# Kernel optimization log

Measured on AMD Instinct MI355X. Metric: run time of the kernel, lower is better.

## Reference

```python
import jax, jax.numpy as jnp
import numpy as np

N_HEAD = 16

def setup_inputs() -> dict:
    key = jax.random.key(0)
    ks = jax.random.split(key, 9)
    B, T, C = 4, 2048, 1024
    s = 0.02
    return {
        "x": jax.random.normal(ks[0], (B, T, C), dtype=jnp.float32),
        "Wq": jax.random.normal(ks[1], (C, C), dtype=jnp.float32) * s,
        "bq": jnp.zeros((C,), dtype=jnp.float32),
        "Wk": jax.random.normal(ks[2], (C, C), dtype=jnp.float32) * s,
        "bk": jnp.zeros((C,), dtype=jnp.float32),
        "Wv": jax.random.normal(ks[3], (C, C), dtype=jnp.float32) * s,
        "bv": jnp.zeros((C,), dtype=jnp.float32),
        "Wo": jax.random.normal(ks[4], (C, C), dtype=jnp.float32) * s,
        "bo": jnp.zeros((C,), dtype=jnp.float32),
    }

def reference(x, Wq, bq, Wk, bk, Wv, bv, Wo, bo):
    B, T, C = x.shape
    H = N_HEAD
    d = C // H
    # QKV projections (Linear: y = x @ W + b), split heads -> [B, H, T, d]
    def proj(W, b):
        return (x @ W + b).reshape(B, T, H, d).transpose(0, 2, 1, 3)
    q = proj(Wq, bq)
    k = proj(Wk, bk)
    v = proj(Wv, bv)
    scale = jnp.float32(d) ** -0.5
    scores = jnp.einsum("bhtd,bhsd->bhts", q, k) * scale  # [B,H,T,T]
    attn = jax.nn.softmax(scores, axis=-1)
    out = jnp.einsum("bhts,bhsd->bhtd", attn, v)  # [B,H,T,d]
    out = out.transpose(0, 2, 1, 3).reshape(B, T, C)
    return out @ Wo + bo
```

## Files before the change

kernel.cpp:

```cpp
#include <hip/hip_runtime.h>
#include <hip/hip_bf16.h>

typedef unsigned short u16;
typedef unsigned int   u32;

typedef __bf16 bf16x8 __attribute__((ext_vector_type(8)));
typedef float  f32x4  __attribute__((ext_vector_type(4)));

#define MFMA16(A, B, C) __builtin_amdgcn_mfma_f32_16x16x32_bf16(A, B, C, 0, 0, 0)

static __device__ __forceinline__ u16 f2bf(float f) {
  union { float f; u32 u; } v; v.f = f;
  u32 r = v.u + 0x7fffu + ((v.u >> 16) & 1u);
  return (u16)(r >> 16);
}

static __device__ __forceinline__ float exp2a(float x) {
  float r; asm("v_exp_f32 %0, %1" : "=v"(r) : "v"(x)); return r;
}
static __device__ __forceinline__ float max3f(float a, float b, float c) {
  float r; asm("v_max3_f32 %0, %1, %2, %3" : "=v"(r) : "v"(a), "v"(b), "v"(c)); return r;
}
static __device__ __forceinline__ u32 cvtpk(float lo, float hi) {
  u32 r; asm("v_cvt_pk_bf16_f32 %0, %1, %2" : "=v"(r) : "v"(lo), "v"(hi)); return r;
}

static __device__ __forceinline__ void async16(const void* g, void* l) {
  __builtin_amdgcn_global_load_lds((const __attribute__((address_space(1))) void*)g,
                                   (__attribute__((address_space(3))) void*)l, 16, 0, 0);
}

static __device__ __forceinline__ int permrow(int r) {
  return (r & 3) | (((r >> 3) & 1) << 2);
}

__global__ __launch_bounds__(256) void cvtx_k(const float* __restrict__ x, u16* __restrict__ xb) {
  size_t i = ((size_t)blockIdx.x * 256 + threadIdx.x) * 4;
  float4 v = *(const float4*)(x + i);
  u32 lo = (u32)f2bf(v.x) | ((u32)f2bf(v.y) << 16);
  u32 hi = (u32)f2bf(v.z) | ((u32)f2bf(v.w) << 16);
  *(uint2*)(xb + i) = make_uint2(lo, hi);
}

__global__ __launch_bounds__(256) void wt_k(const float* __restrict__ Wq, const float* __restrict__ Wk,
                                            const float* __restrict__ Wv, const float* __restrict__ Wo,
                                            u16* __restrict__ WT) {
  const int z = blockIdx.z;
  const float* W = (z == 0) ? Wq : (z == 1) ? Wk : (z == 2) ? Wv : Wo;
  u16* out = WT + (size_t)z * 1048576;
  __shared__ float tile[32][33];
  const int tx = threadIdx.x & 31, ty = threadIdx.x >> 5;
  const int n0 = blockIdx.x * 32, k0 = blockIdx.y * 32;
#pragma unroll
  for (int i = 0; i < 4; i++)
    tile[ty + i * 8][tx] = W[(size_t)(k0 + ty + i * 8) * 1024 + n0 + tx];
  __syncthreads();
#pragma unroll
  for (int i = 0; i < 4; i++)
    out[(size_t)(n0 + ty + i * 8) * 1024 + k0 + tx] = f2bf(tile[tx][ty + i * 8]);
}

template <int MODE>
__global__ __launch_bounds__(256) void gemm_k(const u16* __restrict__ A, const u16* __restrict__ WTall,
                                              const float* __restrict__ b0, const float* __restrict__ b1,
                                              const float* __restrict__ b2,
                                              u16* __restrict__ outb, float* __restrict__ outf) {
  __shared__ u16 As[128 * 32];
  __shared__ u16 Bs[128 * 32];
  const int tid = threadIdx.x;
  const int m0 = blockIdx.x * 128;
  const int n0 = blockIdx.y * 128;
  const int z = blockIdx.z;
  const u16* WT = WTall + (size_t)(MODE == 0 ? z : 3) * 1048576;
  const float* bias = (MODE == 0) ? (z == 0 ? b0 : (z == 1 ? b1 : b2)) : b0;
  const float scl = (MODE == 0 && z == 0) ? 0.18033688011112042f : 1.0f;

  const int lane = tid & 63;
  const int wid = tid >> 6;
  const int wr = wid >> 1, wc = wid & 1;
  const int g = lane >> 4, cc = lane & 15;

  const int srow = tid >> 2;
  const int scol = (tid & 3) * 8;
  const u16* gA0 = A + (size_t)(m0 + srow) * 1024 + scol;
  const u16* gA1 = A + (size_t)(m0 + srow + 64) * 1024 + scol;
  const u16* gB0 = WT + (size_t)(n0 + srow) * 1024 + scol;
  const u16* gB1 = WT + (size_t)(n0 + srow + 64) * 1024 + scol;
  u16* lA0 = &As[tid * 8]; u16* lA1 = &As[2048 + tid * 8];
  u16* lB0 = &Bs[tid * 8]; u16* lB1 = &Bs[2048 + tid * 8];

  f32x4 acc[4][4] = {};

  for (int kb = 0; kb < 1024; kb += 32) {
    __syncthreads();
    async16(gA0 + kb, lA0);
    async16(gA1 + kb, lA1);
    async16(gB0 + kb, lB0);
    async16(gB1 + kb, lB1);
    __syncthreads();
    bf16x8 af[4], bfv[4];
#pragma unroll
    for (int i = 0; i < 4; i++)
      af[i] = *(const bf16x8*)&As[(wr * 64 + i * 16 + cc) * 32 + g * 8];
#pragma unroll
    for (int i = 0; i < 4; i++)
      bfv[i] = *(const bf16x8*)&Bs[(wc * 64 + i * 16 + cc) * 32 + g * 8];
#pragma unroll
    for (int mi = 0; mi < 4; mi++)
#pragma unroll
      for (int ni = 0; ni < 4; ni++)
        acc[mi][ni] = MFMA16(af[mi], bfv[ni], acc[mi][ni]);
  }

#pragma unroll
  for (int mi = 0; mi < 4; mi++) {
#pragma unroll
    for (int ni = 0; ni < 4; ni++) {
      const int n = n0 + wc * 64 + ni * 16 + cc;
      const float bn = bias[n];
      const int mb = m0 + wr * 64 + mi * 16 + g * 4;
      if (MODE == 0) {
        u16* o = outb + (size_t)z * 8388608;
        if (z == 2) {
          u16 h[4];
#pragma unroll
          for (int r = 0; r < 4; r++) h[r] = f2bf(acc[mi][ni][r] + bn);
          const size_t idx = ((size_t)(((mb >> 11) * 16 + (n >> 6)) * 64 + (n & 63))) * 2048 + (mb & 2047);
          *(uint2*)&o[idx] = make_uint2((u32)h[0] | ((u32)h[1] << 16), (u32)h[2] | ((u32)h[3] << 16));
        } else {
#pragma unroll
          for (int r = 0; r < 4; r++) {
            const int m = mb + r;
            const float val = (acc[mi][ni][r] + bn) * scl;
            o[((size_t)((m >> 11) * 16 + (n >> 6)) * 2048 + (m & 2047)) * 64 + (n & 63)] = f2bf(val);
          }
        }
      } else {
#pragma unroll
        for (int r = 0; r < 4; r++)
          outf[(size_t)(mb + r) * 1024 + n] = acc[mi][ni][r] + bn;
      }
    }
  }
}

#define SOFTMAX_GRP(ST, MRUN, O, PF)                                          \
  {                                                                           \
    float pm_ = max3f(max3f(ST[0][0], ST[0][1], ST[0][2]),                    \
                      max3f(ST[0][3], ST[1][0], ST[1][1]),                    \
                      fmaxf(ST[1][2], ST[1][3]));                             \
    if (!__all(pm_ <= MRUN + 8.0f)) {                                         \
      pm_ = fmaxf(pm_, __shfl_xor(pm_, 16));                                  \
      pm_ = fmaxf(pm_, __shfl_xor(pm_, 32));                                  \
      const float mn_ = fmaxf(MRUN, pm_);                                     \
      const float al_ = exp2a(MRUN - mn_);                                    \
      _Pragma("unroll")                                                       \
      for (int r_ = 0; r_ < 4; ++r_) {                                        \
        const float ar_ = __shfl(al_, g * 4 + r_);                            \
        _Pragma("unroll")                                                     \
        for (int t_ = 0; t_ < 5; ++t_) O[t_][r_] *= ar_;                      \
      }                                                                       \
      MRUN = mn_;                                                             \
    }                                                                         \
    const float e0_ = exp2a(ST[0][0] - MRUN), e1_ = exp2a(ST[0][1] - MRUN);   \
    const float e2_ = exp2a(ST[0][2] - MRUN), e3_ = exp2a(ST[0][3] - MRUN);   \
    const float e4_ = exp2a(ST[1][0] - MRUN), e5_ = exp2a(ST[1][1] - MRUN);   \
    const float e6_ = exp2a(ST[1][2] - MRUN), e7_ = exp2a(ST[1][3] - MRUN);   \
    union { u32 u[4]; bf16x8 v; } pu_;                                        \
    pu_.u[0] = cvtpk(e0_, e1_); pu_.u[1] = cvtpk(e2_, e3_);                   \
    pu_.u[2] = cvtpk(e4_, e5_); pu_.u[3] = cvtpk(e6_, e7_);                   \
    PF = pu_.v;                                                               \
  }

#define COMPUTE(BUF)                                                          \
  _Pragma("unroll")                                                           \
  for (int sub = 0; sub < 2; ++sub) {                                         \
    f32x4 stA[2], stB[2];                                                     \
    _Pragma("unroll")                                                         \
    for (int i = 0; i < 2; ++i) {                                             \
      const int row_ = sub * 32 + 8 * a_ + 4 * i + b_;                        \
      const int sl_ = g ^ permrow(row_);                                      \
      bf16x8 k0 = *(const bf16x8*)&Ks[BUF][row_ * 64 + (sl_ << 3)];           \
      bf16x8 k1 = *(const bf16x8*)&Ks[BUF][row_ * 64 + ((sl_ ^ 4) << 3)];     \
      f32x4 t0 = {};                                                          \
      t0 = MFMA16(k0, qfA[0], t0); t0 = MFMA16(k1, qfA[1], t0); stA[i] = t0;  \
      f32x4 t1 = {};                                                          \
      t1 = MFMA16(k0, qfB[0], t1); t1 = MFMA16(k1, qfB[1], t1); stB[i] = t1;  \
    }                                                                         \
    bf16x8 pfA, pfB;                                                          \
    SOFTMAX_GRP(stA, mA, oA, pfA);                                            \
    SOFTMAX_GRP(stB, mB, oB, pfB);                                            \
    _Pragma("unroll")                                                         \
    for (int t = 0; t < 4; ++t) {                                             \
      const int vrow_ = t * 16 + cc;                                          \
      const int sv_ = (sub * 4 + g) ^ permrow(vrow_);                         \
      bf16x8 vf = *(const bf16x8*)&Vs[BUF][vrow_ * 64 + (sv_ << 3)];          \
      oA[t] = MFMA16(pfA, vf, oA[t]);                                         \
      oB[t] = MFMA16(pfB, vf, oB[t]);                                         \
    }                                                                         \
    oA[4] = MFMA16(pfA, vone, oA[4]);                                         \
    oB[4] = MFMA16(pfB, vone, oB[4]);                                         \
  }

#define STEP(BUF, IT)                                                         \
  {                                                                           \
    __syncthreads();                                                          \
    if ((IT) < 31) {                                                          \
      const size_t ko_ = (size_t)((IT) + 1) * 4096;                           \
      const size_t vo_ = (size_t)((IT) + 1) * 64;                             \
      async16(kS0 + ko_, &Ks[BUF ^ 1][tid * 8]);                              \
      async16(kS1 + ko_, &Ks[BUF ^ 1][tid * 8 + 2048]);                       \
      async16(vS0 + vo_, &Vs[BUF ^ 1][tid * 8]);                              \
      async16(vS1 + vo_, &Vs[BUF ^ 1][tid * 8 + 2048]);                       \
    }                                                                         \
    COMPUTE(BUF)                                                              \
  }

__global__ __launch_bounds__(256) void attn_k(const u16* __restrict__ Qg, const u16* __restrict__ Kg,
                                              const u16* __restrict__ Vtg, u16* __restrict__ ctx) {
  __shared__ u16 Ks[2][4096];
  __shared__ u16 Vs[2][4096];
  const int tid = threadIdx.x;
  const int lane = tid & 63;
  const int wid = tid >> 6;
  const int g = lane >> 4, cc = lane & 15;
  const int a_ = cc >> 2, b_ = cc & 3;
  const int bh = blockIdx.y;
  const int q0 = blockIdx.x * 128 + wid * 16;
  const size_t base = (size_t)bh * 131072;

  bf16x8 qfA[2], qfB[2];
#pragma unroll
  for (int c2 = 0; c2 < 2; c2++) {
    qfA[c2] = *(const bf16x8*)(Qg + base + (size_t)(q0 + cc) * 64 + c2 * 32 + g * 8);
    qfB[c2] = *(const bf16x8*)(Qg + base + (size_t)(q0 + 64 + cc) * 64 + c2 * 32 + g * 8);
  }

  bf16x8 vone;
#pragma unroll
  for (int j = 0; j < 8; j++) vone[j] = (__bf16)1.0f;

  float mA = -30000.0f, mB = -30000.0f;
  f32x4 oA[5] = {}, oB[5] = {};

  const int r0 = tid >> 3, r1 = r0 + 32;
  const int slot = tid & 7;
  const int sp0 = slot ^ permrow(r0), sp1 = slot ^ permrow(r1);
  const u16* kS0 = Kg + base + (size_t)r0 * 64 + (sp0 << 3);
  const u16* kS1 = Kg + base + (size_t)r1 * 64 + (sp1 << 3);
  const u16* vS0 = Vtg + base + (size_t)r0 * 2048 + (sp0 << 3);
  const u16* vS1 = Vtg + base + (size_t)r1 * 2048 + (sp1 << 3);

  async16(kS0, &Ks[0][tid * 8]);
  async16(kS1, &Ks[0][tid * 8 + 2048]);
  async16(vS0, &Vs[0][tid * 8]);
  async16(vS1, &Vs[0][tid * 8 + 2048]);

  for (int it = 0; it < 32; it += 2) {
    STEP(0, it)
    STEP(1, it + 1)
  }

  const int b = bh >> 4, h = bh & 15;
#pragma unroll
  for (int r = 0; r < 4; r++) {
    {
      const float inv = __builtin_amdgcn_rcpf(oA[4][r]);
      const int q = q0 + g * 4 + r;
#pragma unroll
      for (int t = 0; t < 4; t++)
        ctx[((size_t)((b * 2048 + q) * 16 + h)) * 64 + t * 16 + cc] = f2bf(oA[t][r] * inv);
    }
    {
      const float inv = __builtin_amdgcn_rcpf(oB[4][r]);
      const int q = q0 + 64 + g * 4 + r;
#pragma unroll
      for (int t = 0; t < 4; t++)
        ctx[((size_t)((b * 2048 + q) * 16 + h)) * 64 + t * 16 + cc] = f2bf(oB[t][r] * inv);
    }
  }
}

extern "C" void kernel_launch(void* const* d_in, const int* in_sizes, int n_in,
                              void* d_out, int out_size, void* d_ws, size_t ws_size,
                              hipStream_t stream) {
  const float* x  = (const float*)d_in[0];
  const float* Wq = (const float*)d_in[1];
  const float* bq = (const float*)d_in[2];
  const float* Wk = (const float*)d_in[3];
  const float* bk = (const float*)d_in[4];
  const float* Wv = (const float*)d_in[5];
  const float* bv = (const float*)d_in[6];
  const float* Wo = (const float*)d_in[7];
  const float* bo = (const float*)d_in[8];
  float* out = (float*)d_out;

  char* w = (char*)d_ws;
  u16* xb   = (u16*)(w);
  u16* WT   = (u16*)(w + (16u << 20));
  u16* QKV  = (u16*)(w + (24u << 20));
  u16* ctxb = (u16*)(w + (72u << 20));

  cvtx_k<<<dim3(8192), dim3(256), 0, stream>>>(x, xb);
  wt_k<<<dim3(32, 32, 4), dim3(256), 0, stream>>>(Wq, Wk, Wv, Wo, WT);
  gemm_k<0><<<dim3(64, 8, 3), dim3(256), 0, stream>>>(xb, WT, bq, bk, bv, QKV, nullptr);
  attn_k<<<dim3(16, 64), dim3(256), 0, stream>>>(QKV, QKV + 8388608, QKV + 2 * 8388608, ctxb);
  gemm_k<1><<<dim3(64, 8, 1), dim3(256), 0, stream>>>(ctxb, WT, bo, nullptr, nullptr, nullptr, out);
}
```

Before: 217.6 us.

## Fold running max into MFMA accumulator init, precompute LDS pointers, XCD-aware block mapping

The running-max subtraction now happens inside the QK^T MFMA: the accumulator starts at -M, so the common path feeds scores straight to exp with no per-element subtraction. Shared-memory K/V fragment addresses are computed once per thread as base pointers with constant offsets, replacing per-iteration permutation math. The grid is flattened and remapped so blocks on the same XCD share a (batch, head), which should improve L2 reuse of K/V. The bf16 products with -M folded in could slightly change numerics.

```diff
diff --git a/kernel.cpp b/kernel.cpp
--- a/kernel.cpp
+++ b/kernel.cpp
@@ -144,28 +144,35 @@
   }
 }
 
-#define SOFTMAX_GRP(ST, MRUN, O, PF)                                          \
+#define SMAX(S0, S1, M, MQ, O, PF)                                            \
   {                                                                           \
-    float pm_ = max3f(max3f(ST[0][0], ST[0][1], ST[0][2]),                    \
-                      max3f(ST[0][3], ST[1][0], ST[1][1]),                    \
-                      fmaxf(ST[1][2], ST[1][3]));                             \
-    if (!__all(pm_ <= MRUN + 8.0f)) {                                         \
+    float pm_ = max3f(max3f(S0[0], S0[1], S0[2]),                             \
+                      max3f(S0[3], S1[0], S1[1]), fmaxf(S1[2], S1[3]));       \
+    float e0_, e1_, e2_, e3_, e4_, e5_, e6_, e7_;                             \
+    if (__builtin_expect(!__all(pm_ <= 8.0f), 0)) {                           \
       pm_ = fmaxf(pm_, __shfl_xor(pm_, 16));                                  \
       pm_ = fmaxf(pm_, __shfl_xor(pm_, 32));                                  \
-      const float mn_ = fmaxf(MRUN, pm_);                                     \
-      const float al_ = exp2a(MRUN - mn_);                                    \
+      const float dm_ = fmaxf(pm_, 0.0f);                                     \
+      const float al_ = exp2a(-dm_);                                          \
       _Pragma("unroll")                                                       \
       for (int r_ = 0; r_ < 4; ++r_) {                                        \
         const float ar_ = __shfl(al_, g * 4 + r_);                            \
         _Pragma("unroll")                                                     \
         for (int t_ = 0; t_ < 5; ++t_) O[t_][r_] *= ar_;                      \
       }                                                                       \
-      MRUN = mn_;                                                             \
+      M += dm_;                                                               \
+      _Pragma("unroll")                                                       \
+      for (int j_ = 0; j_ < 4; ++j_) MQ[j_] = -M;                             \
+      e0_ = exp2a(S0[0] - dm_); e1_ = exp2a(S0[1] - dm_);                     \
+      e2_ = exp2a(S0[2] - dm_); e3_ = exp2a(S0[3] - dm_);                     \
+      e4_ = exp2a(S1[0] - dm_); e5_ = exp2a(S1[1] - dm_);                     \
+      e6_ = exp2a(S1[2] - dm_); e7_ = exp2a(S1[3] - dm_);                     \
+    } else {                                                                  \
+      e0_ = exp2a(S0[0]); e1_ = exp2a(S0[1]);                                 \
+      e2_ = exp2a(S0[2]); e3_ = exp2a(S0[3]);                                 \
+      e4_ = exp2a(S1[0]); e5_ = exp2a(S1[1]);                                 \
+      e6_ = exp2a(S1[2]); e7_ = exp2a(S1[3]);                                 \
     }                                                                         \
-    const float e0_ = exp2a(ST[0][0] - MRUN), e1_ = exp2a(ST[0][1] - MRUN);   \
-    const float e2_ = exp2a(ST[0][2] - MRUN), e3_ = exp2a(ST[0][3] - MRUN);   \
-    const float e4_ = exp2a(ST[1][0] - MRUN), e5_ = exp2a(ST[1][1] - MRUN);   \
-    const float e6_ = exp2a(ST[1][2] - MRUN), e7_ = exp2a(ST[1][3] - MRUN);   \
     union { u32 u[4]; bf16x8 v; } pu_;                                        \
     pu_.u[0] = cvtpk(e0_, e1_); pu_.u[1] = cvtpk(e2_, e3_);                   \
     pu_.u[2] = cvtpk(e4_, e5_); pu_.u[3] = cvtpk(e6_, e7_);                   \
@@ -175,26 +182,21 @@
 #define COMPUTE(BUF)                                                          \
   _Pragma("unroll")                                                           \
   for (int sub = 0; sub < 2; ++sub) {                                         \
-    f32x4 stA[2], stB[2];                                                     \
-    _Pragma("unroll")                                                         \
-    for (int i = 0; i < 2; ++i) {                                             \
-      const int row_ = sub * 32 + 8 * a_ + 4 * i + b_;                        \
-      const int sl_ = g ^ permrow(row_);                                      \
-      bf16x8 k0 = *(const bf16x8*)&Ks[BUF][row_ * 64 + (sl_ << 3)];           \
-      bf16x8 k1 = *(const bf16x8*)&Ks[BUF][row_ * 64 + ((sl_ ^ 4) << 3)];     \
-      f32x4 t0 = {};                                                          \
-      t0 = MFMA16(k0, qfA[0], t0); t0 = MFMA16(k1, qfA[1], t0); stA[i] = t0;  \
-      f32x4 t1 = {};                                                          \
-      t1 = MFMA16(k0, qfB[0], t1); t1 = MFMA16(k1, qfB[1], t1); stB[i] = t1;  \
-    }                                                                         \
+    const u16* pV_ = sub ? pV1 : pV0;                                         \
+    bf16x8 k00 = *(const bf16x8*)(pK0 + (BUF)*4096 + sub*2048 + 0*256);       \
+    bf16x8 k01 = *(const bf16x8*)(pK1 + (BUF)*4096 + sub*2048 + 0*256);       \
+    bf16x8 k10 = *(const bf16x8*)(pK0 + (BUF)*4096 + sub*2048 + 1*256);       \
+    bf16x8 k11 = *(const bf16x8*)(pK1 + (BUF)*4096 + sub*2048 + 1*256);       \
+    f32x4 sA0 = MFMA16(k00, qfA[0], mqA); sA0 = MFMA16(k01, qfA[1], sA0);     \
+    f32x4 sB0 = MFMA16(k00, qfB[0], mqB); sB0 = MFMA16(k01, qfB[1], sB0);     \
+    f32x4 sA1 = MFMA16(k10, qfA[0], mqA); sA1 = MFMA16(k11, qfA[1], sA1);     \
+    f32x4 sB1 = MFMA16(k10, qfB[0], mqB); sB1 = MFMA16(k11, qfB[1], sB1);     \
     bf16x8 pfA, pfB;                                                          \
-    SOFTMAX_GRP(stA, mA, oA, pfA);                                            \
-    SOFTMAX_GRP(stB, mB, oB, pfB);                                            \
+    SMAX(sA0, sA1, mA, mqA, oA, pfA);                                         \
+    SMAX(sB0, sB1, mB, mqB, oB, pfB);                                         \
     _Pragma("unroll")                                                         \
     for (int t = 0; t < 4; ++t) {                                             \
-      const int vrow_ = t * 16 + cc;                                          \
-      const int sv_ = (sub * 4 + g) ^ permrow(vrow_);                         \
-      bf16x8 vf = *(const bf16x8*)&Vs[BUF][vrow_ * 64 + (sv_ << 3)];          \
+      bf16x8 vf = *(const bf16x8*)(pV_ + (BUF)*4096 + t*1024);                \
       oA[t] = MFMA16(pfA, vf, oA[t]);                                         \
       oB[t] = MFMA16(pfB, vf, oB[t]);                                         \
     }                                                                         \
@@ -208,25 +210,28 @@
     if ((IT) < 31) {                                                          \
       const size_t ko_ = (size_t)((IT) + 1) * 4096;                           \
       const size_t vo_ = (size_t)((IT) + 1) * 64;                             \
-      async16(kS0 + ko_, &Ks[BUF ^ 1][tid * 8]);                              \
-      async16(kS1 + ko_, &Ks[BUF ^ 1][tid * 8 + 2048]);                       \
-      async16(vS0 + vo_, &Vs[BUF ^ 1][tid * 8]);                              \
-      async16(vS1 + vo_, &Vs[BUF ^ 1][tid * 8 + 2048]);                       \
+      async16(kS0 + ko_, &Ks[((BUF) ^ 1) * 4096 + tid * 8]);                  \
+      async16(kS1 + ko_, &Ks[((BUF) ^ 1) * 4096 + tid * 8 + 2048]);           \
+      async16(vS0 + vo_, &Vs[((BUF) ^ 1) * 4096 + tid * 8]);                  \
+      async16(vS1 + vo_, &Vs[((BUF) ^ 1) * 4096 + tid * 8 + 2048]);           \
     }                                                                         \
     COMPUTE(BUF)                                                              \
   }
 
 __global__ __launch_bounds__(256) void attn_k(const u16* __restrict__ Qg, const u16* __restrict__ Kg,
                                               const u16* __restrict__ Vtg, u16* __restrict__ ctx) {
-  __shared__ u16 Ks[2][4096];
-  __shared__ u16 Vs[2][4096];
+  __shared__ u16 Ks[8192];
+  __shared__ u16 Vs[8192];
   const int tid = threadIdx.x;
   const int lane = tid & 63;
   const int wid = tid >> 6;
   const int g = lane >> 4, cc = lane & 15;
   const int a_ = cc >> 2, b_ = cc & 3;
-  const int bh = blockIdx.y;
-  const int q0 = blockIdx.x * 128 + wid * 16;
+
+  const int bid = blockIdx.x;
+  const int xcd = bid & 7, tt = bid >> 3;
+  const int bh = xcd * 8 + (tt >> 4);
+  const int q0 = (tt & 15) * 128 + wid * 16;
   const size_t base = (size_t)bh * 131072;
 
   bf16x8 qfA[2], qfB[2];
@@ -240,8 +245,17 @@
 #pragma unroll
   for (int j = 0; j < 8; j++) vone[j] = (__bf16)1.0f;
 
-  float mA = -30000.0f, mB = -30000.0f;
+  float mA = 0.0f, mB = 0.0f;
+  f32x4 mqA = {}, mqB = {};
   f32x4 oA[5] = {}, oB[5] = {};
+
+  const int cK = b_ | ((a_ & 1) << 2);
+  const int slK = g ^ cK;
+  const u16* pK0 = &Ks[(8 * a_ + b_) * 64 + (slK << 3)];
+  const u16* pK1 = &Ks[(8 * a_ + b_) * 64 + ((slK ^ 4) << 3)];
+  const int cV = b_ | (((cc >> 3) & 1) << 2);
+  const u16* pV0 = &Vs[cc * 64 + ((g ^ cV) << 3)];
+  const u16* pV1 = &Vs[cc * 64 + (((4 + g) ^ cV) << 3)];
 
   const int r0 = tid >> 3, r1 = r0 + 32;
   const int slot = tid & 7;
@@ -251,10 +265,10 @@
   const u16* vS0 = Vtg + base + (size_t)r0 * 2048 + (sp0 << 3);
   const u16* vS1 = Vtg + base + (size_t)r1 * 2048 + (sp1 << 3);
 
-  async16(kS0, &Ks[0][tid * 8]);
-  async16(kS1, &Ks[0][tid * 8 + 2048]);
-  async16(vS0, &Vs[0][tid * 8]);
-  async16(vS1, &Vs[0][tid * 8 + 2048]);
+  async16(kS0, &Ks[tid * 8]);
+  async16(kS1, &Ks[tid * 8 + 2048]);
+  async16(vS0, &Vs[tid * 8]);
+  async16(vS1, &Vs[tid * 8 + 2048]);
 
   for (int it = 0; it < 32; it += 2) {
     STEP(0, it)
@@ -304,6 +318,6 @@
   cvtx_k<<<dim3(8192), dim3(256), 0, stream>>>(x, xb);
   wt_k<<<dim3(32, 32, 4), dim3(256), 0, stream>>>(Wq, Wk, Wv, Wo, WT);
   gemm_k<0><<<dim3(64, 8, 3), dim3(256), 0, stream>>>(xb, WT, bq, bk, bv, QKV, nullptr);
-  attn_k<<<dim3(16, 64), dim3(256), 0, stream>>>(QKV, QKV + 8388608, QKV + 2 * 8388608, ctxb);
+  attn_k<<<dim3(1024), dim3(256), 0, stream>>>(QKV, QKV + 8388608, QKV + 2 * 8388608, ctxb);
   gemm_k<1><<<dim3(64, 8, 1), dim3(256), 0, stream>>>(ctxb, WT, bo, nullptr, nullptr, nullptr, out);
 }
```

New measurement: 263.0 us. +20.9%, slower.
